# Kernel tuning notes

Measured on AMD Instinct MI355X. Metric: run time of the kernel, lower is better.

## Reference

```python
import jax, jax.numpy as jnp
import numpy as np

N, E, D, H, ED = 50000, 800000, 128, 16, 16
TAU = 0.5

def _seg_sum(data, ids, n):
    return jax.ops.segment_sum(data, ids, num_segments=n)

def gcn_conv(x, src, dst, ew, W, b, n):
    # PyG-style GCNConv with added self-loops (weight 1) and symmetric normalization
    xw = x @ W                                   # [n, out]
    deg = _seg_sum(ew, dst, n) + 1.0             # in-degree incl. self-loop
    dinv = jax.lax.rsqrt(deg)
    norm = dinv[src] * ew * dinv[dst]            # [E]
    out = _seg_sum(xw[src] * norm[:, None], dst, n)
    out = out + xw * (dinv * dinv)[:, None]      # self-loop message
    return out + b

def layer_norm(x, g, b, eps=1e-5):
    mu = jnp.mean(x, -1, keepdims=True)
    var = jnp.mean((x - mu) ** 2, -1, keepdims=True)
    return (x - mu) * jax.lax.rsqrt(var + eps) * g + b

def gumbel_hard(logits, u, tau):
    # F.gumbel_softmax(hard=True) with straight-through estimator
    g = -jnp.log(-jnp.log(u + 1e-10) + 1e-10)
    y = jax.nn.softmax((logits + g) / tau, axis=-1)
    hard = jax.nn.one_hot(jnp.argmax(y, -1), y.shape[-1], dtype=y.dtype)
    return hard + y - jax.lax.stop_gradient(y)

def action_net(x, src, dst, w1, b1, w2, b2, n):
    ones = jnp.ones((src.shape[0],), x.dtype)
    h = jax.nn.relu(gcn_conv(x, src, dst, ones, w1, b1, n))
    return gcn_conv(h, src, dst, ones, w2, b2, n)    # [n, 2]

def setup_inputs():
    key = jax.random.key(0)
    ks = jax.random.split(key, 12)
    p = lambda k, s: (0.02 * jax.random.normal(k, s)).astype(jnp.float32)
    return dict(
        x=jax.random.normal(ks[0], (N, D), jnp.float32),
        edge_index=jax.random.randint(ks[1], (2, E), 0, N, jnp.int32),
        edge_attr=jax.random.normal(ks[2], (E, ED), jnp.float32),
        u_in=jax.random.uniform(ks[3], (N, 2), jnp.float32),
        u_out=jax.random.uniform(ks[4], (N, 2), jnp.float32),
        ln_g=jnp.ones((D,), jnp.float32), ln_b=jnp.zeros((D,), jnp.float32),
        conv_w=p(ks[5], (D, D)), conv_b=jnp.zeros((D,), jnp.float32),
        ep_w=p(ks[6], (ED, D)), ep_b=jnp.zeros((D,), jnp.float32),
        ia1_w=p(ks[7], (D, H)), ia1_b=jnp.zeros((H,), jnp.float32),
        ia2_w=p(ks[8], (H, 2)), ia2_b=jnp.zeros((2,), jnp.float32),
        oa1_w=p(ks[9], (D, H)), oa1_b=jnp.zeros((H,), jnp.float32),
        oa2_w=p(ks[10], (H, 2)), oa2_b=jnp.zeros((2,), jnp.float32),
    )

def reference(x, edge_index, edge_attr, u_in, u_out, ln_g, ln_b, conv_w, conv_b,
              ep_w, ep_b, ia1_w, ia1_b, ia2_w, ia2_b, oa1_w, oa1_b, oa2_w, oa2_b):
    src, dst = edge_index[0], edge_index[1]
    # edge_proj (dropout is identity in eval mode)
    edge_features = jax.nn.relu(edge_attr @ ep_w + ep_b)      # [E, D]
    xn = layer_norm(x, ln_g, ln_b)
    in_logits = action_net(xn, src, dst, ia1_w, ia1_b, ia2_w, ia2_b, N)
    out_logits = action_net(xn, src, dst, oa1_w, oa1_b, oa2_w, oa2_b, N)
    in_probs = gumbel_hard(in_logits, u_in, TAU)
    out_probs = gumbel_hard(out_logits, u_out, TAU)
    edge_weight = in_probs[dst, 0] * out_probs[src, 0]        # [E]
    out = gcn_conv(xn, src, dst, edge_weight, conv_w, conv_b, N)
    out = out + _seg_sum(edge_features, dst, N)
    return jax.nn.relu(out)
```

## Files before the change

kernel.cpp:

```cpp
#include <hip/hip_runtime.h>
#include <hip/hip_bf16.h>

#define DD 128
#define HH 16
#define SCAN_B 1024

__global__ void ln_kernel(const float* __restrict__ x, const float* __restrict__ g,
                          const float* __restrict__ b, float* __restrict__ xn, int n_nodes) {
  int w = (blockIdx.x * blockDim.x + threadIdx.x) >> 6;
  int lane = threadIdx.x & 63;
  if (w >= n_nodes) return;
  const float* xr = x + (size_t)w * DD;
  float a0 = xr[lane], a1 = xr[lane + 64];
  float s = a0 + a1;
  #pragma unroll
  for (int o = 32; o > 0; o >>= 1) s += __shfl_down(s, o);
  s = __shfl(s, 0);
  float mu = s * (1.0f / DD);
  float d0 = a0 - mu, d1 = a1 - mu;
  float v = d0 * d0 + d1 * d1;
  #pragma unroll
  for (int o = 32; o > 0; o >>= 1) v += __shfl_down(v, o);
  v = __shfl(v, 0);
  float rstd = rsqrtf(v * (1.0f / DD) + 1e-5f);
  float* xo = xn + (size_t)w * DD;
  xo[lane]      = d0 * rstd * g[lane] + b[lane];
  xo[lane + 64] = d1 * rstd * g[lane + 64] + b[lane + 64];
}

__global__ __launch_bounds__(256) void proj1_kernel(const float* __restrict__ xn,
    const float* __restrict__ ia1_w, const float* __restrict__ oa1_w,
    float* __restrict__ xw_a, int n_nodes) {
  __shared__ __align__(16) float wl[DD * 32];
  for (int i = threadIdx.x; i < DD * HH; i += 256) {
    int dd = i >> 4, jj = i & 15;
    wl[dd * 32 + jj]      = ia1_w[i];
    wl[dd * 32 + 16 + jj] = oa1_w[i];
  }
  __syncthreads();
  int t = blockIdx.x * blockDim.x + threadIdx.x;
  int n = t >> 5, j = t & 31;
  if (n >= n_nodes) return;
  const float* xr = xn + (size_t)n * DD;
  float acc = 0.f;
  #pragma unroll 8
  for (int d = 0; d < DD; ++d) acc = fmaf(xr[d], wl[d * 32 + j], acc);
  xw_a[(size_t)n * 32 + j] = acc;
}

__global__ void degcnt_kernel(const int* __restrict__ dst, int* __restrict__ deg, int n_edges) {
  int e = blockIdx.x * blockDim.x + threadIdx.x;
  if (e < n_edges) atomicAdd(&deg[dst[e]], 1);
}

__global__ __launch_bounds__(SCAN_B) void scan1_kernel(const int* __restrict__ deg,
    int* __restrict__ rs, int* __restrict__ partials, int n_nodes) {
  __shared__ int sm[SCAN_B];
  int i = blockIdx.x * SCAN_B + threadIdx.x;
  int v = (i < n_nodes) ? deg[i] : 0;
  sm[threadIdx.x] = v;
  __syncthreads();
  for (int o = 1; o < SCAN_B; o <<= 1) {
    int t = (threadIdx.x >= o) ? sm[threadIdx.x - o] : 0;
    __syncthreads();
    sm[threadIdx.x] += t;
    __syncthreads();
  }
  if (i < n_nodes) rs[i] = sm[threadIdx.x] - v;
  if (threadIdx.x == SCAN_B - 1) partials[blockIdx.x] = sm[threadIdx.x];
}

__global__ __launch_bounds__(SCAN_B) void scan2_kernel(int* __restrict__ partials, int nb) {
  __shared__ int sm[SCAN_B];
  int v = (threadIdx.x < nb) ? partials[threadIdx.x] : 0;
  sm[threadIdx.x] = v;
  __syncthreads();
  for (int o = 1; o < SCAN_B; o <<= 1) {
    int t = (threadIdx.x >= o) ? sm[threadIdx.x - o] : 0;
    __syncthreads();
    sm[threadIdx.x] += t;
    __syncthreads();
  }
  if (threadIdx.x < nb) partials[threadIdx.x] = sm[threadIdx.x] - v;
}

__global__ __launch_bounds__(SCAN_B) void scan3_kernel(int* __restrict__ rs,
    const int* __restrict__ partials, int n_nodes) {
  int i = blockIdx.x * SCAN_B + threadIdx.x;
  if (i < n_nodes) rs[i] += partials[blockIdx.x];
}

__global__ void fill_kernel(const int* __restrict__ src, const int* __restrict__ dst,
    int* __restrict__ rs, int* __restrict__ csr_eid, int* __restrict__ csr_src, int n_edges) {
  int e = blockIdx.x * blockDim.x + threadIdx.x;
  if (e >= n_edges) return;
  int d = dst[e];
  int pos = atomicAdd(&rs[d], 1);
  csr_eid[pos] = e;
  csr_src[pos] = src[e];
}

__global__ void dinva_kernel(const int* __restrict__ deg, float* __restrict__ dinv, int n_nodes) {
  int i = blockIdx.x * blockDim.x + threadIdx.x;
  if (i < n_nodes) dinv[i] = rsqrtf((float)deg[i] + 1.0f);
}

__global__ __launch_bounds__(256) void agg1_kernel(const int* __restrict__ rs,
    const int* __restrict__ deg, const int* __restrict__ csr_src,
    const float* __restrict__ xw_a, const float* __restrict__ dinva,
    const float* __restrict__ ia1_b, const float* __restrict__ oa1_b,
    const float* __restrict__ ia2_w, const float* __restrict__ oa2_w,
    float* __restrict__ xw2_a, int n_nodes) {
  int t = blockIdx.x * blockDim.x + threadIdx.x;
  int node = t >> 5, j = t & 31;
  if (node >= n_nodes) return;
  int dg = deg[node];
  int st = rs[node] - dg;
  float acc = 0.f;
  for (int i = 0; i < dg; ++i) {
    int s = csr_src[st + i];
    acc = fmaf(xw_a[(size_t)s * 32 + j], dinva[s], acc);
  }
  float di = dinva[node];
  float bias = (j < 16) ? ia1_b[j] : oa1_b[j - 16];
  float h = fmaxf(acc * di + xw_a[(size_t)node * 32 + j] * di * di + bias, 0.f);
  float w0 = (j < 16) ? ia2_w[j * 2 + 0] : oa2_w[(j - 16) * 2 + 0];
  float w1 = (j < 16) ? ia2_w[j * 2 + 1] : oa2_w[(j - 16) * 2 + 1];
  float p0 = h * w0, p1 = h * w1;
  #pragma unroll
  for (int o = 1; o < 16; o <<= 1) { p0 += __shfl_xor(p0, o); p1 += __shfl_xor(p1, o); }
  if ((j & 15) == 0) {
    int k = j >> 4;
    xw2_a[(size_t)node * 4 + k * 2 + 0] = p0;
    xw2_a[(size_t)node * 4 + k * 2 + 1] = p1;
  }
}

__global__ void agg2_kernel(const int* __restrict__ rs, const int* __restrict__ deg,
    const int* __restrict__ csr_src, const float* __restrict__ xw2_a,
    const float* __restrict__ dinva, const float* __restrict__ ia2_b,
    const float* __restrict__ oa2_b, const float* __restrict__ u_in,
    const float* __restrict__ u_out, float* __restrict__ fin, float* __restrict__ fout,
    int n_nodes) {
  int node = blockIdx.x * blockDim.x + threadIdx.x;
  if (node >= n_nodes) return;
  int dg = deg[node];
  int st = rs[node] - dg;
  float a0 = 0.f, a1 = 0.f, a2 = 0.f, a3 = 0.f;
  for (int i = 0; i < dg; ++i) {
    int s = csr_src[st + i];
    float ds = dinva[s];
    float4 v = *(const float4*)&xw2_a[(size_t)s * 4];
    a0 = fmaf(v.x, ds, a0); a1 = fmaf(v.y, ds, a1);
    a2 = fmaf(v.z, ds, a2); a3 = fmaf(v.w, ds, a3);
  }
  float di = dinva[node], sw = di * di;
  float4 self = *(const float4*)&xw2_a[(size_t)node * 4];
  float li0 = a0 * di + self.x * sw + ia2_b[0];
  float li1 = a1 * di + self.y * sw + ia2_b[1];
  float lo0 = a2 * di + self.z * sw + oa2_b[0];
  float lo1 = a3 * di + self.w * sw + oa2_b[1];
  float gi0 = -logf(-logf(u_in[(size_t)node * 2 + 0] + 1e-10f) + 1e-10f);
  float gi1 = -logf(-logf(u_in[(size_t)node * 2 + 1] + 1e-10f) + 1e-10f);
  float go0 = -logf(-logf(u_out[(size_t)node * 2 + 0] + 1e-10f) + 1e-10f);
  float go1 = -logf(-logf(u_out[(size_t)node * 2 + 1] + 1e-10f) + 1e-10f);
  fin[node]  = (li0 + gi0 >= li1 + gi1) ? 1.f : 0.f;
  fout[node] = (lo0 + go0 >= lo1 + go1) ? 1.f : 0.f;
}

__global__ void cdeg_kernel(const int* __restrict__ rs, const int* __restrict__ deg,
    const int* __restrict__ csr_src, const float* __restrict__ fin,
    const float* __restrict__ fout, float* __restrict__ dinvc, int n_nodes) {
  int node = blockIdx.x * blockDim.x + threadIdx.x;
  if (node >= n_nodes) return;
  int dg = deg[node];
  int st = rs[node] - dg;
  float c = 0.f;
  if (fin[node] != 0.f) {
    for (int i = 0; i < dg; ++i) c += (fout[csr_src[st + i]] != 0.f) ? 1.f : 0.f;
  }
  dinvc[node] = rsqrtf(c + 1.0f);
}

#define GEMM_ROWS 64
__global__ __launch_bounds__(256) void gemm_kernel(const float* __restrict__ xn,
    const float* __restrict__ W, float* __restrict__ xwc, int n_nodes) {
  __shared__ __align__(16) float wl[DD * DD];
  for (int i = threadIdx.x * 4; i < DD * DD; i += 256 * 4)
    *(float4*)&wl[i] = *(const float4*)&W[i];
  __syncthreads();
  int c4 = (threadIdx.x & 31) * 4;
  int r0 = threadIdx.x >> 5;
  int base = blockIdx.x * GEMM_ROWS;
  for (int r = r0; r < GEMM_ROWS; r += 8) {
    int n = base + r;
    if (n >= n_nodes) break;
    const float* xr = xn + (size_t)n * DD;
    float4 acc = {0.f, 0.f, 0.f, 0.f};
    #pragma unroll 4
    for (int d = 0; d < DD; ++d) {
      float xv = xr[d];
      float4 w = *(const float4*)&wl[d * DD + c4];
      acc.x = fmaf(xv, w.x, acc.x);
      acc.y = fmaf(xv, w.y, acc.y);
      acc.z = fmaf(xv, w.z, acc.z);
      acc.w = fmaf(xv, w.w, acc.w);
    }
    *(float4*)&xwc[(size_t)n * DD + c4] = acc;
  }
}

__global__ __launch_bounds__(256) void kbig_kernel(const int* __restrict__ rs,
    const int* __restrict__ deg, const int* __restrict__ csr_src,
    const int* __restrict__ csr_eid, const float* __restrict__ ea,
    const float* __restrict__ ep_w, const float* __restrict__ ep_b,
    const float* __restrict__ xwc, const float* __restrict__ dinvc,
    const float* __restrict__ fin, const float* __restrict__ fout,
    const float* __restrict__ conv_b, float* __restrict__ out, int n_nodes) {
  __shared__ __align__(16) float wl[HH * DD];
  __shared__ float bl[DD];
  for (int i = threadIdx.x; i < HH * DD; i += 256) wl[i] = ep_w[i];
  if (threadIdx.x < DD) bl[threadIdx.x] = ep_b[threadIdx.x];
  __syncthreads();
  int t = blockIdx.x * blockDim.x + threadIdx.x;
  int node = t >> 7, j = t & 127;
  if (node >= n_nodes) return;
  int dg = deg[node];
  int st = rs[node] - dg;
  float fd = fin[node];
  float dj = dinvc[node];
  float aed = 0.f, acv = 0.f;
  for (int i = 0; i < dg; ++i) {
    int e = csr_eid[st + i];
    int s = csr_src[st + i];
    const float4* ear = (const float4*)(ea + (size_t)e * HH);
    float4 e0 = ear[0], e1 = ear[1], e2 = ear[2], e3 = ear[3];
    float m = bl[j];
    m = fmaf(e0.x, wl[0 * DD + j], m);
    m = fmaf(e0.y, wl[1 * DD + j], m);
    m = fmaf(e0.z, wl[2 * DD + j], m);
    m = fmaf(e0.w, wl[3 * DD + j], m);
    m = fmaf(e1.x, wl[4 * DD + j], m);
    m = fmaf(e1.y, wl[5 * DD + j], m);
    m = fmaf(e1.z, wl[6 * DD + j], m);
    m = fmaf(e1.w, wl[7 * DD + j], m);
    m = fmaf(e2.x, wl[8 * DD + j], m);
    m = fmaf(e2.y, wl[9 * DD + j], m);
    m = fmaf(e2.z, wl[10 * DD + j], m);
    m = fmaf(e2.w, wl[11 * DD + j], m);
    m = fmaf(e3.x, wl[12 * DD + j], m);
    m = fmaf(e3.y, wl[13 * DD + j], m);
    m = fmaf(e3.z, wl[14 * DD + j], m);
    m = fmaf(e3.w, wl[15 * DD + j], m);
    aed += fmaxf(m, 0.f);
    if (fd != 0.f) {
      float fs = fout[s];
      if (fs != 0.f) acv = fmaf(xwc[(size_t)s * DD + j], dinvc[s], acv);
    }
  }
  float v = aed + acv * dj + xwc[(size_t)node * DD + j] * dj * dj + conv_b[j];
  out[(size_t)node * DD + j] = fmaxf(v, 0.f);
}

extern "C" void kernel_launch(void* const* d_in, const int* in_sizes, int n_in,
                              void* d_out, int out_size, void* d_ws, size_t ws_size,
                              hipStream_t stream) {
  const float* x      = (const float*)d_in[0];
  const int*   eidx   = (const int*)d_in[1];
  const float* ea     = (const float*)d_in[2];
  const float* u_in   = (const float*)d_in[3];
  const float* u_out  = (const float*)d_in[4];
  const float* ln_g   = (const float*)d_in[5];
  const float* ln_b   = (const float*)d_in[6];
  const float* conv_w = (const float*)d_in[7];
  const float* conv_b = (const float*)d_in[8];
  const float* ep_w   = (const float*)d_in[9];
  const float* ep_b   = (const float*)d_in[10];
  const float* ia1_w  = (const float*)d_in[11];
  const float* ia1_b  = (const float*)d_in[12];
  const float* ia2_w  = (const float*)d_in[13];
  const float* ia2_b  = (const float*)d_in[14];
  const float* oa1_w  = (const float*)d_in[15];
  const float* oa1_b  = (const float*)d_in[16];
  const float* oa2_w  = (const float*)d_in[17];
  const float* oa2_b  = (const float*)d_in[18];

  const int n = in_sizes[0] / DD;
  const int E = in_sizes[1] / 2;
  const int* src = eidx;
  const int* dst = eidx + E;

  float* ws = (float*)d_ws;
  float* xn    = ws;
  float* xw_a  = xn + (size_t)n * 128;
  float* xw2_a = xw_a + (size_t)n * 32;
  float* dinva = xw2_a + (size_t)n * 4;
  float* xwc   = dinva + n;
  int* deg_i   = (int*)(xwc + (size_t)n * 128);
  int* rs      = deg_i + n;
  int* partials= rs + n;
  int* csr_eid = partials + 1024;
  int* csr_src = csr_eid + E;
  float* fin   = xw_a;
  float* fout  = xw_a + n;
  float* dinvc = xw_a + 2 * (size_t)n;

  float* out = (float*)d_out;

  hipMemsetAsync(deg_i, 0, (size_t)n * sizeof(int), stream);

  const int B = 256;
  const int nb = (n + SCAN_B - 1) / SCAN_B;

  ln_kernel<<<(n * 64 + B - 1) / B, B, 0, stream>>>(x, ln_g, ln_b, xn, n);
  proj1_kernel<<<(n * 32 + B - 1) / B, B, 0, stream>>>(xn, ia1_w, oa1_w, xw_a, n);
  degcnt_kernel<<<(E + B - 1) / B, B, 0, stream>>>(dst, deg_i, E);
  scan1_kernel<<<nb, SCAN_B, 0, stream>>>(deg_i, rs, partials, n);
  scan2_kernel<<<1, SCAN_B, 0, stream>>>(partials, nb);
  scan3_kernel<<<nb, SCAN_B, 0, stream>>>(rs, partials, n);
  dinva_kernel<<<(n + B - 1) / B, B, 0, stream>>>(deg_i, dinva, n);
  fill_kernel<<<(E + B - 1) / B, B, 0, stream>>>(src, dst, rs, csr_eid, csr_src, E);
  agg1_kernel<<<(n * 32 + B - 1) / B, B, 0, stream>>>(rs, deg_i, csr_src, xw_a, dinva,
                                                      ia1_b, oa1_b, ia2_w, oa2_w, xw2_a, n);
  agg2_kernel<<<(n + B - 1) / B, B, 0, stream>>>(rs, deg_i, csr_src, xw2_a, dinva,
                                                 ia2_b, oa2_b, u_in, u_out, fin, fout, n);
  cdeg_kernel<<<(n + B - 1) / B, B, 0, stream>>>(rs, deg_i, csr_src, fin, fout, dinvc, n);
  gemm_kernel<<<(n + GEMM_ROWS - 1) / GEMM_ROWS, B, 0, stream>>>(xn, conv_w, xwc, n);
  kbig_kernel<<<((size_t)n * DD + B - 1) / B, B, 0, stream>>>(rs, deg_i, csr_src, csr_eid,
      ea, ep_w, ep_b, xwc, dinvc, fin, fout, conv_b, out, n);
}
```

Before: 790.8 us.

## Precompute edge MLP with bf16 MFMA and parallelize per-node gathers

Adds an MFMA-based kernel that computes relu(edge_attr @ ep_w + b) for all edges in CSR order and stores the result as bf16 in the workspace. The main aggregation kernel then only sums these precomputed rows per node, with 64 lanes each handling two columns, instead of recomputing the 16-wide projection 128 times per edge. agg2 and cdeg now use 16 lanes per node with shuffle reductions in place of one serial thread per node. The cost is an extra E×128 bf16 buffer written and read back, bf16 rounding of edge features, and a fallback to the old fused kernel when the workspace is too small.

```diff
diff --git a/kernel.cpp b/kernel.cpp
--- a/kernel.cpp
+++ b/kernel.cpp
@@ -4,6 +4,10 @@
 #define DD 128
 #define HH 16
 #define SCAN_B 1024
+#define TPW 8
+
+typedef __bf16 bf16x8 __attribute__((ext_vector_type(8)));
+typedef float f32x4 __attribute__((ext_vector_type(4)));
 
 __global__ void ln_kernel(const float* __restrict__ x, const float* __restrict__ g,
                           const float* __restrict__ b, float* __restrict__ xn, int n_nodes) {
@@ -142,44 +146,55 @@
     const float* __restrict__ oa2_b, const float* __restrict__ u_in,
     const float* __restrict__ u_out, float* __restrict__ fin, float* __restrict__ fout,
     int n_nodes) {
-  int node = blockIdx.x * blockDim.x + threadIdx.x;
+  int t = blockIdx.x * blockDim.x + threadIdx.x;
+  int node = t >> 4, l = t & 15;
   if (node >= n_nodes) return;
   int dg = deg[node];
   int st = rs[node] - dg;
   float a0 = 0.f, a1 = 0.f, a2 = 0.f, a3 = 0.f;
-  for (int i = 0; i < dg; ++i) {
+  for (int i = l; i < dg; i += 16) {
     int s = csr_src[st + i];
     float ds = dinva[s];
     float4 v = *(const float4*)&xw2_a[(size_t)s * 4];
     a0 = fmaf(v.x, ds, a0); a1 = fmaf(v.y, ds, a1);
     a2 = fmaf(v.z, ds, a2); a3 = fmaf(v.w, ds, a3);
   }
-  float di = dinva[node], sw = di * di;
-  float4 self = *(const float4*)&xw2_a[(size_t)node * 4];
-  float li0 = a0 * di + self.x * sw + ia2_b[0];
-  float li1 = a1 * di + self.y * sw + ia2_b[1];
-  float lo0 = a2 * di + self.z * sw + oa2_b[0];
-  float lo1 = a3 * di + self.w * sw + oa2_b[1];
-  float gi0 = -logf(-logf(u_in[(size_t)node * 2 + 0] + 1e-10f) + 1e-10f);
-  float gi1 = -logf(-logf(u_in[(size_t)node * 2 + 1] + 1e-10f) + 1e-10f);
-  float go0 = -logf(-logf(u_out[(size_t)node * 2 + 0] + 1e-10f) + 1e-10f);
-  float go1 = -logf(-logf(u_out[(size_t)node * 2 + 1] + 1e-10f) + 1e-10f);
-  fin[node]  = (li0 + gi0 >= li1 + gi1) ? 1.f : 0.f;
-  fout[node] = (lo0 + go0 >= lo1 + go1) ? 1.f : 0.f;
+  #pragma unroll
+  for (int o = 1; o < 16; o <<= 1) {
+    a0 += __shfl_xor(a0, o); a1 += __shfl_xor(a1, o);
+    a2 += __shfl_xor(a2, o); a3 += __shfl_xor(a3, o);
+  }
+  if (l == 0) {
+    float di = dinva[node], sw = di * di;
+    float4 self = *(const float4*)&xw2_a[(size_t)node * 4];
+    float li0 = a0 * di + self.x * sw + ia2_b[0];
+    float li1 = a1 * di + self.y * sw + ia2_b[1];
+    float lo0 = a2 * di + self.z * sw + oa2_b[0];
+    float lo1 = a3 * di + self.w * sw + oa2_b[1];
+    float gi0 = -logf(-logf(u_in[(size_t)node * 2 + 0] + 1e-10f) + 1e-10f);
+    float gi1 = -logf(-logf(u_in[(size_t)node * 2 + 1] + 1e-10f) + 1e-10f);
+    float go0 = -logf(-logf(u_out[(size_t)node * 2 + 0] + 1e-10f) + 1e-10f);
+    float go1 = -logf(-logf(u_out[(size_t)node * 2 + 1] + 1e-10f) + 1e-10f);
+    fin[node]  = (li0 + gi0 >= li1 + gi1) ? 1.f : 0.f;
+    fout[node] = (lo0 + go0 >= lo1 + go1) ? 1.f : 0.f;
+  }
 }
 
 __global__ void cdeg_kernel(const int* __restrict__ rs, const int* __restrict__ deg,
     const int* __restrict__ csr_src, const float* __restrict__ fin,
     const float* __restrict__ fout, float* __restrict__ dinvc, int n_nodes) {
-  int node = blockIdx.x * blockDim.x + threadIdx.x;
+  int t = blockIdx.x * blockDim.x + threadIdx.x;
+  int node = t >> 4, l = t & 15;
   if (node >= n_nodes) return;
   int dg = deg[node];
   int st = rs[node] - dg;
   float c = 0.f;
   if (fin[node] != 0.f) {
-    for (int i = 0; i < dg; ++i) c += (fout[csr_src[st + i]] != 0.f) ? 1.f : 0.f;
-  }
-  dinvc[node] = rsqrtf(c + 1.0f);
+    for (int i = l; i < dg; i += 16) c += (fout[csr_src[st + i]] != 0.f) ? 1.f : 0.f;
+  }
+  #pragma unroll
+  for (int o = 1; o < 16; o <<= 1) c += __shfl_xor(c, o);
+  if (l == 0) dinvc[node] = rsqrtf(c + 1.0f);
 }
 
 #define GEMM_ROWS 64
@@ -210,7 +225,97 @@
   }
 }
 
+__global__ __launch_bounds__(256) void mlp_kernel(const int* __restrict__ csr_eid,
+    const float* __restrict__ ea, const float* __restrict__ ep_w,
+    const float* __restrict__ ep_b, __bf16* __restrict__ ef, int n_edges) {
+  int l = threadIdx.x & 63;
+  int wave_g = (blockIdx.x * 256 + threadIdx.x) >> 6;
+  int tile0 = wave_g * TPW;
+  int col = l & 15;
+  int kg = l >> 4;
+  int k0 = kg * 8;
+  bool a_active = (k0 < HH);
+  bf16x8 bfr[8];
+  float bias[8];
+  #pragma unroll
+  for (int nt = 0; nt < 8; ++nt) {
+    int j = nt * 16 + col;
+    bf16x8 bb;
+    #pragma unroll
+    for (int i = 0; i < 8; ++i) {
+      int k = k0 + i;
+      bb[i] = (__bf16)((k < HH) ? ep_w[k * DD + j] : 0.f);
+    }
+    bfr[nt] = bb;
+    bias[nt] = ep_b[j];
+  }
+  for (int t = 0; t < TPW; ++t) {
+    int pos0 = (tile0 + t) * 16;
+    if (pos0 >= n_edges) return;
+    int apos = pos0 + col;
+    int eid = csr_eid[(apos < n_edges) ? apos : (n_edges - 1)];
+    bf16x8 afr = {};
+    if (a_active) {
+      const float4* er = (const float4*)(ea + (size_t)eid * HH + k0);
+      float4 f0 = er[0], f1 = er[1];
+      afr[0] = (__bf16)f0.x; afr[1] = (__bf16)f0.y;
+      afr[2] = (__bf16)f0.z; afr[3] = (__bf16)f0.w;
+      afr[4] = (__bf16)f1.x; afr[5] = (__bf16)f1.y;
+      afr[6] = (__bf16)f1.z; afr[7] = (__bf16)f1.w;
+    }
+    #pragma unroll
+    for (int nt = 0; nt < 8; ++nt) {
+      f32x4 d = {0.f, 0.f, 0.f, 0.f};
+      d = __builtin_amdgcn_mfma_f32_16x16x32_bf16(afr, bfr[nt], d, 0, 0, 0);
+      int j = nt * 16 + col;
+      #pragma unroll
+      for (int r = 0; r < 4; ++r) {
+        int pos = pos0 + kg * 4 + r;
+        if (pos < n_edges)
+          ef[(size_t)pos * DD + j] = (__bf16)fmaxf(d[r] + bias[nt], 0.f);
+      }
+    }
+  }
+}
+
 __global__ __launch_bounds__(256) void kbig_kernel(const int* __restrict__ rs,
+    const int* __restrict__ deg, const int* __restrict__ csr_src,
+    const __bf16* __restrict__ ef, const float* __restrict__ xwc,
+    const float* __restrict__ dinvc, const float* __restrict__ fin,
+    const float* __restrict__ fout, const float* __restrict__ conv_b,
+    float* __restrict__ out, int n_nodes) {
+  int node = (blockIdx.x * blockDim.x + threadIdx.x) >> 6;
+  int l = threadIdx.x & 63;
+  if (node >= n_nodes) return;
+  int dg = deg[node];
+  int st = rs[node] - dg;
+  float fd = fin[node];
+  float dj = dinvc[node];
+  float a0 = 0.f, a1 = 0.f, c0 = 0.f, c1 = 0.f;
+  for (int i = 0; i < dg; ++i) {
+    int pos = st + i;
+    unsigned u = *(const unsigned*)(ef + (size_t)pos * DD + 2 * l);
+    a0 += __uint_as_float(u << 16);
+    a1 += __uint_as_float(u & 0xffff0000u);
+    if (fd != 0.f) {
+      int s = csr_src[pos];
+      if (fout[s] != 0.f) {
+        float2 w = *(const float2*)(xwc + (size_t)s * DD + 2 * l);
+        float ds = dinvc[s];
+        c0 = fmaf(w.x, ds, c0);
+        c1 = fmaf(w.y, ds, c1);
+      }
+    }
+  }
+  float2 selfw = *(const float2*)(xwc + (size_t)node * DD + 2 * l);
+  float2 cb = *(const float2*)(conv_b + 2 * l);
+  float o0 = a0 + c0 * dj + selfw.x * dj * dj + cb.x;
+  float o1 = a1 + c1 * dj + selfw.y * dj * dj + cb.y;
+  float2 res = {fmaxf(o0, 0.f), fmaxf(o1, 0.f)};
+  *(float2*)(out + (size_t)node * DD + 2 * l) = res;
+}
+
+__global__ __launch_bounds__(256) void kbig_fused_kernel(const int* __restrict__ rs,
     const int* __restrict__ deg, const int* __restrict__ csr_src,
     const int* __restrict__ csr_eid, const float* __restrict__ ea,
     const float* __restrict__ ep_w, const float* __restrict__ ep_b,
@@ -236,26 +341,17 @@
     const float4* ear = (const float4*)(ea + (size_t)e * HH);
     float4 e0 = ear[0], e1 = ear[1], e2 = ear[2], e3 = ear[3];
     float m = bl[j];
-    m = fmaf(e0.x, wl[0 * DD + j], m);
-    m = fmaf(e0.y, wl[1 * DD + j], m);
-    m = fmaf(e0.z, wl[2 * DD + j], m);
-    m = fmaf(e0.w, wl[3 * DD + j], m);
-    m = fmaf(e1.x, wl[4 * DD + j], m);
-    m = fmaf(e1.y, wl[5 * DD + j], m);
-    m = fmaf(e1.z, wl[6 * DD + j], m);
-    m = fmaf(e1.w, wl[7 * DD + j], m);
-    m = fmaf(e2.x, wl[8 * DD + j], m);
-    m = fmaf(e2.y, wl[9 * DD + j], m);
-    m = fmaf(e2.z, wl[10 * DD + j], m);
-    m = fmaf(e2.w, wl[11 * DD + j], m);
-    m = fmaf(e3.x, wl[12 * DD + j], m);
-    m = fmaf(e3.y, wl[13 * DD + j], m);
-    m = fmaf(e3.z, wl[14 * DD + j], m);
-    m = fmaf(e3.w, wl[15 * DD + j], m);
+    m = fmaf(e0.x, wl[0 * DD + j], m); m = fmaf(e0.y, wl[1 * DD + j], m);
+    m = fmaf(e0.z, wl[2 * DD + j], m); m = fmaf(e0.w, wl[3 * DD + j], m);
+    m = fmaf(e1.x, wl[4 * DD + j], m); m = fmaf(e1.y, wl[5 * DD + j], m);
+    m = fmaf(e1.z, wl[6 * DD + j], m); m = fmaf(e1.w, wl[7 * DD + j], m);
+    m = fmaf(e2.x, wl[8 * DD + j], m); m = fmaf(e2.y, wl[9 * DD + j], m);
+    m = fmaf(e2.z, wl[10 * DD + j], m); m = fmaf(e2.w, wl[11 * DD + j], m);
+    m = fmaf(e3.x, wl[12 * DD + j], m); m = fmaf(e3.y, wl[13 * DD + j], m);
+    m = fmaf(e3.z, wl[14 * DD + j], m); m = fmaf(e3.w, wl[15 * DD + j], m);
     aed += fmaxf(m, 0.f);
     if (fd != 0.f) {
-      float fs = fout[s];
-      if (fs != 0.f) acv = fmaf(xwc[(size_t)s * DD + j], dinvc[s], acv);
+      if (fout[s] != 0.f) acv = fmaf(xwc[(size_t)s * DD + j], dinvc[s], acv);
     }
   }
   float v = aed + acv * dj + xwc[(size_t)node * DD + j] * dj * dj + conv_b[j];
@@ -301,11 +397,15 @@
   int* partials= rs + n;
   int* csr_eid = partials + 1024;
   int* csr_src = csr_eid + E;
+  __bf16* ef   = (__bf16*)(csr_src + E);
   float* fin   = xw_a;
   float* fout  = xw_a + n;
   float* dinvc = xw_a + 2 * (size_t)n;
 
   float* out = (float*)d_out;
+
+  size_t need = ((size_t)n * 295 + 2 * (size_t)E + 1024) * 4 + (size_t)E * DD * 2;
+  bool big_ws = ws_size >= need;
 
   hipMemsetAsync(deg_i, 0, (size_t)n * sizeof(int), stream);
 
@@ -322,10 +422,20 @@
   fill_kernel<<<(E + B - 1) / B, B, 0, stream>>>(src, dst, rs, csr_eid, csr_src, E);
   agg1_kernel<<<(n * 32 + B - 1) / B, B, 0, stream>>>(rs, deg_i, csr_src, xw_a, dinva,
                                                       ia1_b, oa1_b, ia2_w, oa2_w, xw2_a, n);
-  agg2_kernel<<<(n + B - 1) / B, B, 0, stream>>>(rs, deg_i, csr_src, xw2_a, dinva,
-                                                 ia2_b, oa2_b, u_in, u_out, fin, fout, n);
-  cdeg_kernel<<<(n + B - 1) / B, B, 0, stream>>>(rs, deg_i, csr_src, fin, fout, dinvc, n);
+  agg2_kernel<<<(n * 16 + B - 1) / B, B, 0, stream>>>(rs, deg_i, csr_src, xw2_a, dinva,
+                                                      ia2_b, oa2_b, u_in, u_out, fin, fout, n);
+  cdeg_kernel<<<(n * 16 + B - 1) / B, B, 0, stream>>>(rs, deg_i, csr_src, fin, fout, dinvc, n);
   gemm_kernel<<<(n + GEMM_ROWS - 1) / GEMM_ROWS, B, 0, stream>>>(xn, conv_w, xwc, n);
-  kbig_kernel<<<((size_t)n * DD + B - 1) / B, B, 0, stream>>>(rs, deg_i, csr_src, csr_eid,
-      ea, ep_w, ep_b, xwc, dinvc, fin, fout, conv_b, out, n);
-}
+
+  if (big_ws) {
+    int tiles = (E + 15) / 16;
+    int nwaves = (tiles + TPW - 1) / TPW;
+    int nblocks = (nwaves + 3) / 4;
+    mlp_kernel<<<nblocks, B, 0, stream>>>(csr_eid, ea, ep_w, ep_b, ef, E);
+    kbig_kernel<<<((size_t)n * 64 + B - 1) / B, B, 0, stream>>>(rs, deg_i, csr_src, ef,
+        xwc, dinvc, fin, fout, conv_b, out, n);
+  } else {
+    kbig_fused_kernel<<<((size_t)n * DD + B - 1) / B, B, 0, stream>>>(rs, deg_i, csr_src,
+        csr_eid, ea, ep_w, ep_b, xwc, dinvc, fin, fout, conv_b, out, n);
+  }
+}
```

New measurement: 773.6 us. 2.2% less time.
